# Kernel optimization log

Measured on AMD Instinct MI355X. Metric: run time of the kernel, lower is better.

Reference implementation:

```python
import jax, jax.numpy as jnp
import numpy as np

P = 7  # output_size


def _axis_weights(start, length, dim):
    """Per-roi 1D interpolation matrix A [R, P, dim] such that the roi_align
    output separates as out = Ay @ fm @ Ax^T (torchvision roi_align,
    aligned=False, sampling_ratio=-1 i.e. adaptive ceil(bin) samples)."""
    S = int(np.ceil(dim / P))  # max samples per bin (rois lie inside the image)
    bin_sz = length / P                               # [R]
    grid = jnp.ceil(length / P).astype(jnp.int32)     # adaptive samples per bin, [R]
    g = grid.astype(jnp.float32)[:, None, None]       # [R,1,1]
    s = jnp.arange(S, dtype=jnp.float32)              # [S]
    ph = jnp.arange(P, dtype=jnp.float32)             # [P]
    # sample coordinate: start + ph*bin + (s+0.5)*bin/grid  -> [R,P,S]
    coord = (start[:, None, None] + ph[None, :, None] * bin_sz[:, None, None]
             + (s[None, None, :] + 0.5) * bin_sz[:, None, None] / g)
    valid = (coord >= -1.0) & (coord <= dim)
    c = jnp.maximum(coord, 0.0)
    low = jnp.floor(c).astype(jnp.int32)
    hi_clamp = low >= dim - 1
    low = jnp.where(hi_clamp, dim - 1, low)
    high = jnp.where(hi_clamp, dim - 1, low + 1)
    cv = jnp.where(hi_clamp, low.astype(jnp.float32), c)
    l = cv - low.astype(jnp.float32)
    smask = (s[None, None, :] < g) & valid            # mask unused samples
    w = smask.astype(jnp.float32) / g                 # 1/count split per axis
    w_low = (1.0 - l) * w
    w_high = l * w
    R = start.shape[0]
    r_idx = jnp.arange(R)[:, None, None]
    p_idx = jnp.arange(P)[None, :, None]
    A = jnp.zeros((R, P, dim), dtype=jnp.float32)
    A = A.at[r_idx, p_idx, low].add(w_low)
    A = A.at[r_idx, p_idx, high].add(w_high)
    return A


def _roi_align(fm, rois):
    # fm: [C,H,W]; rois: [R,4] = (x1,y1,x2,y2); spatial_scale=1.0
    C, H, W = fm.shape
    x1, y1, x2, y2 = rois[:, 0], rois[:, 1], rois[:, 2], rois[:, 3]
    roi_w = jnp.maximum(x2 - x1, 1.0)
    roi_h = jnp.maximum(y2 - y1, 1.0)
    Ay = _axis_weights(y1, roi_h, H)                  # [R,P,H]
    Ax = _axis_weights(x1, roi_w, W)                  # [R,P,W]
    tmp = jnp.einsum('rph,chw->rcpw', Ay, fm)         # [R,C,P,W]
    return jnp.einsum('rcpw,rqw->rcpq', tmp, Ax)      # [R,C,P,P]


def _per_image(fm, b, g):
    # fm: [C,H,W], b: [N,4] boxes, g: [M,4] gt boxes
    N, M = b.shape[0], g.shape[0]
    # context boxes: union (min of mins, max of maxes) of every (box, gt) pair
    x1 = jnp.minimum(b[:, None, 0], g[None, :, 0])
    y1 = jnp.minimum(b[:, None, 1], g[None, :, 1])
    x2 = jnp.maximum(b[:, None, 2], g[None, :, 2])
    y2 = jnp.maximum(b[:, None, 3], g[None, :, 3])
    ctx = jnp.stack([x1, y1, x2, y2], axis=-1).reshape(N * M, 4)
    feats = _roi_align(fm, jnp.concatenate([b, ctx], axis=0))  # [N+N*M,C,P,P]
    box_f = feats[:N]
    ctx_mean = feats[N:].reshape(N, M, feats.shape[1], P, P).mean(axis=1)
    return box_f + ctx_mean                            # [N,C,P,P]


def setup_inputs() -> dict:
    key = jax.random.key(0)
    B, C, H, W, N, M = 2, 256, 56, 56, 64, 8
    k1, k2, k3, k4, k5 = jax.random.split(key, 5)
    feature_map = jax.random.normal(k1, (B, C, H, W), dtype=jnp.float32)
    # boxes inside the feature map, max side 0.35*H so adaptive grid <= ceil(H/7)
    b_xy1 = jax.random.uniform(k2, (B, N, 2), minval=0.0, maxval=0.64 * H)
    b_wh = jax.random.uniform(k3, (B, N, 2), minval=4.0, maxval=0.35 * H)
    boxes = jnp.concatenate([b_xy1, b_xy1 + b_wh], axis=-1).astype(jnp.float32)
    g_xy1 = jax.random.uniform(k4, (B, M, 2), minval=0.0, maxval=0.64 * H)
    g_wh = jax.random.uniform(k5, (B, M, 2), minval=4.0, maxval=0.35 * H)
    gt_boxes = jnp.concatenate([g_xy1, g_xy1 + g_wh], axis=-1).astype(jnp.float32)
    return {"feature_map": feature_map, "boxes": boxes, "gt_boxes": gt_boxes}


def reference(feature_map, boxes, gt_boxes):
    # returns [B, N, C, P, P] (stacked version of the per-image list output)
    return jax.vmap(_per_image)(feature_map, boxes, gt_boxes)
```

## Files before the change

### kernel.cpp

```cpp
#include <hip/hip_runtime.h>

#define B_ 2
#define C_ 256
#define H_ 56
#define W_ 56
#define N_ 64
#define M_ 8
#define P_ 7
#define R_ (N_ + N_*M_)
#define BR_ (B_*R_)
#define Y2_ (H_/2)
#define Y4_ (H_/4)
#define SCTX_ 4
#define JPN_ (1 + (M_)*SCTX_)
#define WROW_ 8

typedef _Float16 half2v __attribute__((ext_vector_type(2)));

#if __has_builtin(__builtin_amdgcn_fdot2)
#define FDOT2(a, b, c) __builtin_amdgcn_fdot2((a), (b), (c), false)
#else
static __device__ __forceinline__ float FDOT2(half2v a, half2v b, float c) {
    return fmaf((float)a.x, (float)b.x, fmaf((float)a.y, (float)b.y, c));
}
#endif

#define F_FMT4 0
#define N_FMT4 (B_*Y4_*W_*C_*2)
#define F_OUTS (F_FMT4 + N_FMT4)
#define N_OUTS (B_*N_*49*C_)
#define WS_ELEMS (F_OUTS + N_OUTS)

#define PREP_T (B_*Y4_*2)
#define PREP_N (PREP_T + 784)

__global__ __launch_bounds__(256) void k_prep(const float* __restrict__ fm,
                                              float* __restrict__ ws_f) {
    int bid = blockIdx.x;
    int tid = (int)threadIdx.x;

    if (bid < PREP_T) {
        int xh = bid & 1;
        int y4 = (bid >> 1) % Y4_;
        int b  = bid / (2 * Y4_);
        int c  = tid;
        int x0 = xh * (W_ / 2);
        const float* base = fm + (((size_t)b * C_ + c) * H_ + 4 * y4) * W_ + x0;
        const float4* r0 = (const float4*)(base);
        const float4* r1 = (const float4*)(base + W_);
        const float4* r2 = (const float4*)(base + 2 * W_);
        const float4* r3 = (const float4*)(base + 3 * W_);
        uint2* dst = (uint2*)ws_f + (((size_t)b * Y4_ + y4) * W_ + x0) * (size_t)C_ + c;
#pragma unroll
        for (int x4 = 0; x4 < W_ / 8; ++x4) {
            float4 a = r0[x4], e = r1[x4], f = r2[x4], g = r3[x4];
            half2v lo, hi; uint2 o;
            lo.x = (_Float16)a.x; lo.y = (_Float16)e.x;
            hi.x = (_Float16)f.x; hi.y = (_Float16)g.x;
            o.x = __builtin_bit_cast(unsigned int, lo);
            o.y = __builtin_bit_cast(unsigned int, hi);
            dst[(x4 * 4 + 0) * C_] = o;
            lo.x = (_Float16)a.y; lo.y = (_Float16)e.y;
            hi.x = (_Float16)f.y; hi.y = (_Float16)g.y;
            o.x = __builtin_bit_cast(unsigned int, lo);
            o.y = __builtin_bit_cast(unsigned int, hi);
            dst[(x4 * 4 + 1) * C_] = o;
            lo.x = (_Float16)a.z; lo.y = (_Float16)e.z;
            hi.x = (_Float16)f.z; hi.y = (_Float16)g.z;
            o.x = __builtin_bit_cast(unsigned int, lo);
            o.y = __builtin_bit_cast(unsigned int, hi);
            dst[(x4 * 4 + 2) * C_] = o;
            lo.x = (_Float16)a.w; lo.y = (_Float16)e.w;
            hi.x = (_Float16)f.w; hi.y = (_Float16)g.w;
            o.x = __builtin_bit_cast(unsigned int, lo);
            o.y = __builtin_bit_cast(unsigned int, hi);
            dst[(x4 * 4 + 3) * C_] = o;
        }
        return;
    }

    {
        int t = (bid - PREP_T) * 256 + tid;
        float4 z = {0.0f, 0.0f, 0.0f, 0.0f};
        float4* dst = (float4*)(ws_f + F_OUTS);
        dst[t * 2]     = z;
        dst[t * 2 + 1] = z;
    }
}

__global__ __launch_bounds__(256, 4) void k_main(const float* __restrict__ ws_f,
                                                 const float* __restrict__ boxes,
                                                 const float* __restrict__ gt,
                                                 float* __restrict__ outs) {
    __shared__ float        s_wyf[H_][WROW_];
    __shared__ unsigned int s_wy2[Y2_ * WROW_];
    __shared__ float        s_ax[W_][WROW_];

    int bid = blockIdx.x;
    int j   = bid % JPN_;
    int n   = (bid / JPN_) & (N_ - 1);
    int b   = bid / (JPN_ * N_);
    int k, s;
    if (j == 0) { k = 0; s = 0; }
    else        { k = 1 + ((j - 1) >> 2); s = (j - 1) & 3; }
    int tid  = (int)threadIdx.x;
    int lane = tid & 63;
    int rg   = tid >> 6;
    int c    = rg * 64 + lane;

    const float* bp = boxes + ((size_t)b * N_ + n) * 4;
    float bx1, by1, bx2, by2;
    if (k == 0) {
        bx1 = bp[0]; by1 = bp[1]; bx2 = bp[2]; by2 = bp[3];
    } else {
        const float* gp = gt + ((size_t)b * M_ + (k - 1)) * 4;
        bx1 = fminf(bp[0], gp[0]); by1 = fminf(bp[1], gp[1]);
        bx2 = fmaxf(bp[2], gp[2]); by2 = fmaxf(bp[3], gp[3]);
    }
    float rw = fmaxf(bx2 - bx1, 1.0f);
    float rh = fmaxf(by2 - by1, 1.0f);

    for (int e = tid; e < H_ * WROW_; e += 256) ((float*)s_wyf)[e] = 0.0f;
    for (int e = tid; e < W_ * WROW_; e += 256) ((float*)s_ax)[e] = 0.0f;
    __syncthreads();

    if (tid < P_) {
        int p = tid;
        float bin = rh / 7.0f;
        float gf  = ceilf(bin);
        int   g   = (int)gf;
        float ivg = 1.0f / gf;
        float start = by1 + (float)p * bin;
        for (int ss = 0; ss < g; ++ss) {
            float coord = start + ((float)ss + 0.5f) * bin * ivg;
            if (coord < -1.0f || coord > (float)H_) continue;
            float cc = fmaxf(coord, 0.0f);
            int low = (int)floorf(cc);
            int high; float l;
            if (low >= H_ - 1) { low = H_ - 1; high = H_ - 1; l = 0.0f; }
            else               { high = low + 1; l = cc - (float)low; }
            s_wyf[low][p]  += (1.0f - l) * ivg;
            s_wyf[high][p] += l * ivg;
        }
    } else if (tid >= 64 && tid < 64 + P_) {
        int p = tid - 64;
        float bin = rw / 7.0f;
        float gf  = ceilf(bin);
        int   g   = (int)gf;
        float ivg = 1.0f / gf;
        float fs  = (k == 0) ? ivg : ivg * (1.0f / (float)M_);
        float start = bx1 + (float)p * bin;
        for (int ss = 0; ss < g; ++ss) {
            float coord = start + ((float)ss + 0.5f) * bin * ivg;
            if (coord < -1.0f || coord > (float)W_) continue;
            float cc = fmaxf(coord, 0.0f);
            int low = (int)floorf(cc);
            int high; float l;
            if (low >= W_ - 1) { low = W_ - 1; high = W_ - 1; l = 0.0f; }
            else               { high = low + 1; l = cc - (float)low; }
            s_ax[low][p]  += (1.0f - l) * fs;
            s_ax[high][p] += l * fs;
        }
    }
    __syncthreads();

    if (tid < Y2_ * WROW_) {
        int q2 = tid >> 3, col = tid & 7;
        half2v h;
        if (col < P_) { h.x = (_Float16)s_wyf[2 * q2][col]; h.y = (_Float16)s_wyf[2 * q2 + 1][col]; }
        else          { h.x = (_Float16)0.0f; h.y = (_Float16)0.0f; }
        s_wy2[tid] = __builtin_bit_cast(unsigned int, h);
    }
    __syncthreads();

    int xlo = min(max((int)floorf(fmaxf(bx1, 0.0f)), 0), W_ - 1);
    int xhi = min(max((int)floorf(bx1 + rw) + 1, 0), W_ - 1) + 1;
    int ylo = min(max((int)floorf(fmaxf(by1, 0.0f)), 0), H_ - 1);
    int yhi = min(max((int)floorf(by1 + rh) + 1, 0), H_ - 1) + 1;
    int xs, xe;
    if (k == 0) { xs = xlo; xe = xhi; }
    else {
        int cw = (xhi - xlo + SCTX_ - 1) >> 2;
        xs = xlo + s * cw;
        xe = min(xs + cw, xhi);
    }
    if (xs >= xe) return;

    int ylo4 = ylo >> 2;
    int yhi4 = (yhi + 3) >> 2;

    const uint2* f4 = (const uint2*)ws_f + (size_t)b * (Y4_ * W_ * C_);

    float acc[49];
#pragma unroll
    for (int q = 0; q < 49; ++q) acc[q] = 0.0f;
    int live = 0;

    for (int x = xs; x < xe; x += 4) {
        float cs[4][P_];
#pragma unroll
        for (int i = 0; i < 4; ++i)
#pragma unroll
            for (int py = 0; py < P_; ++py) cs[i][py] = 0.0f;

        const uint2* cp = f4 + ((size_t)(ylo4 * W_ + x)) * C_ + c;
        for (int y4 = ylo4; y4 < yhi4; ++y4) {
            uint2 d0 = cp[0];
            uint2 d1 = cp[C_];
            uint2 d2 = cp[2 * C_];
            uint2 d3 = cp[3 * C_];
            uint4 wa0 = *(const uint4*)&s_wy2[(2 * y4) * WROW_];
            uint4 wb0 = *(const uint4*)&s_wy2[(2 * y4) * WROW_ + 4];
            uint4 wa1 = *(const uint4*)&s_wy2[(2 * y4 + 1) * WROW_];
            uint4 wb1 = *(const uint4*)&s_wy2[(2 * y4 + 1) * WROW_ + 4];
            half2v w0[7], w1[7];
            w0[0] = __builtin_bit_cast(half2v, wa0.x);
            w0[1] = __builtin_bit_cast(half2v, wa0.y);
            w0[2] = __builtin_bit_cast(half2v, wa0.z);
            w0[3] = __builtin_bit_cast(half2v, wa0.w);
            w0[4] = __builtin_bit_cast(half2v, wb0.x);
            w0[5] = __builtin_bit_cast(half2v, wb0.y);
            w0[6] = __builtin_bit_cast(half2v, wb0.z);
            w1[0] = __builtin_bit_cast(half2v, wa1.x);
            w1[1] = __builtin_bit_cast(half2v, wa1.y);
            w1[2] = __builtin_bit_cast(half2v, wa1.z);
            w1[3] = __builtin_bit_cast(half2v, wa1.w);
            w1[4] = __builtin_bit_cast(half2v, wb1.x);
            w1[5] = __builtin_bit_cast(half2v, wb1.y);
            w1[6] = __builtin_bit_cast(half2v, wb1.z);
            half2v v0a = __builtin_bit_cast(half2v, d0.x);
            half2v v0b = __builtin_bit_cast(half2v, d0.y);
            half2v v1a = __builtin_bit_cast(half2v, d1.x);
            half2v v1b = __builtin_bit_cast(half2v, d1.y);
            half2v v2a = __builtin_bit_cast(half2v, d2.x);
            half2v v2b = __builtin_bit_cast(half2v, d2.y);
            half2v v3a = __builtin_bit_cast(half2v, d3.x);
            half2v v3b = __builtin_bit_cast(half2v, d3.y);
#pragma unroll
            for (int py = 0; py < P_; ++py) {
                cs[0][py] = FDOT2(w1[py], v0b, FDOT2(w0[py], v0a, cs[0][py]));
                cs[1][py] = FDOT2(w1[py], v1b, FDOT2(w0[py], v1a, cs[1][py]));
                cs[2][py] = FDOT2(w1[py], v2b, FDOT2(w0[py], v2a, cs[2][py]));
                cs[3][py] = FDOT2(w1[py], v3b, FDOT2(w0[py], v3a, cs[3][py]));
            }
            cp += W_ * C_;
        }

#pragma unroll
        for (int i = 0; i < 4; ++i) {
            if (x + i < xe) {
                float av[8];
                *(float4*)(&av[0]) = *(const float4*)&s_ax[x + i][0];
                *(float4*)(&av[4]) = *(const float4*)&s_ax[x + i][4];
#pragma unroll
                for (int px = 0; px < P_; ++px) {
                    float w = av[px];
                    if (w != 0.0f) {
                        live |= 1 << px;
#pragma unroll
                        for (int py = 0; py < P_; ++py)
                            acc[py * P_ + px] = fmaf(w, cs[i][py], acc[py * P_ + px]);
                    }
                }
            }
        }
    }

    float* os = outs + ((size_t)b * N_ + n) * (49 * C_) + c;
#pragma unroll
    for (int px = 0; px < P_; ++px) {
        if (live & (1 << px)) {
#pragma unroll
            for (int py = 0; py < P_; ++py)
                atomicAdd(os + (py * P_ + px) * C_, acc[py * P_ + px]);
        }
    }
}

__global__ __launch_bounds__(256) void k_final(const float* __restrict__ outs,
                                               float* __restrict__ out) {
    __shared__ float t[49 * 257];
    int bn  = blockIdx.x;
    int tid = (int)threadIdx.x;
    const float* src = outs + (size_t)bn * (49 * C_);
    for (int e = tid; e < 49 * C_; e += 256) {
        int q = e >> 8, c = e & 255;
        t[q * 257 + c] = src[e];
    }
    __syncthreads();
    float* dst = out + (size_t)bn * (C_ * 49);
    for (int e = tid; e < C_ * 49; e += 256) {
        int c = e / 49, q = e % 49;
        dst[e] = t[q * 257 + c];
    }
}

extern "C" void kernel_launch(void* const* d_in, const int* in_sizes, int n_in,
                              void* d_out, int out_size, void* d_ws, size_t ws_size,
                              hipStream_t stream) {
    const float* fm    = (const float*)d_in[0];
    const float* boxes = (const float*)d_in[1];
    const float* gt    = (const float*)d_in[2];
    float* ws_f = (float*)d_ws;
    float* out  = (float*)d_out;
    float* outs = ws_f + F_OUTS;

    k_prep<<<PREP_N, 256, 0, stream>>>(fm, ws_f);
    k_main<<<B_ * N_ * JPN_, 256, 0, stream>>>(ws_f, boxes, gt, outs);
    k_final<<<B_ * N_, 256, 0, stream>>>(outs, out);
}
```

Measured before the change: 149.8 us.

## Use persistent work-stealing main kernel and finer-grained prep and final kernels

The main kernel becomes a persistent grid of 2048 blocks that pull job indices from a global atomic counter, which is reset in the prep kernel. The per-roi weight build now spreads the sample loop over 8 threads per output bin using shared-memory atomics. The prep kernel is split into 7 x-chunks per row group, and the final transpose is split into 4 channel groups per roi, to raise parallelism in both. The aim is better load balance across uneven roi sizes and less launch tail, at the cost of atomic-counter contention and extra block-level syncs per job.

```diff
diff --git a/kernel.cpp b/kernel.cpp
--- a/kernel.cpp
+++ b/kernel.cpp
@@ -13,6 +13,8 @@
 #define Y4_ (H_/4)
 #define SCTX_ 4
 #define JPN_ (1 + (M_)*SCTX_)
+#define NJOBS_ (B_*N_*JPN_)
+#define PERSIST_ 2048
 #define WROW_ 8
 
 typedef _Float16 half2v __attribute__((ext_vector_type(2)));
@@ -29,9 +31,10 @@
 #define N_FMT4 (B_*Y4_*W_*C_*2)
 #define F_OUTS (F_FMT4 + N_FMT4)
 #define N_OUTS (B_*N_*49*C_)
-#define WS_ELEMS (F_OUTS + N_OUTS)
-
-#define PREP_T (B_*Y4_*2)
+#define F_CNT  (F_OUTS + N_OUTS)
+#define WS_ELEMS (F_CNT + 64)
+
+#define PREP_T (B_*Y4_*7)
 #define PREP_N (PREP_T + 784)
 
 __global__ __launch_bounds__(256) void k_prep(const float* __restrict__ fm,
@@ -40,47 +43,40 @@
     int tid = (int)threadIdx.x;
 
     if (bid < PREP_T) {
-        int xh = bid & 1;
-        int y4 = (bid >> 1) % Y4_;
-        int b  = bid / (2 * Y4_);
+        int xc = bid % 7;
+        int y4 = (bid / 7) % Y4_;
+        int b  = bid / (7 * Y4_);
         int c  = tid;
-        int x0 = xh * (W_ / 2);
+        int x0 = xc * 8;
         const float* base = fm + (((size_t)b * C_ + c) * H_ + 4 * y4) * W_ + x0;
-        const float4* r0 = (const float4*)(base);
-        const float4* r1 = (const float4*)(base + W_);
-        const float4* r2 = (const float4*)(base + 2 * W_);
-        const float4* r3 = (const float4*)(base + 3 * W_);
+        float4 a0 = *(const float4*)(base);
+        float4 a1 = *(const float4*)(base + 4);
+        float4 e0 = *(const float4*)(base + W_);
+        float4 e1 = *(const float4*)(base + W_ + 4);
+        float4 f0 = *(const float4*)(base + 2 * W_);
+        float4 f1 = *(const float4*)(base + 2 * W_ + 4);
+        float4 g0 = *(const float4*)(base + 3 * W_);
+        float4 g1 = *(const float4*)(base + 3 * W_ + 4);
+        float r0[8] = {a0.x, a0.y, a0.z, a0.w, a1.x, a1.y, a1.z, a1.w};
+        float r1[8] = {e0.x, e0.y, e0.z, e0.w, e1.x, e1.y, e1.z, e1.w};
+        float r2[8] = {f0.x, f0.y, f0.z, f0.w, f1.x, f1.y, f1.z, f1.w};
+        float r3[8] = {g0.x, g0.y, g0.z, g0.w, g1.x, g1.y, g1.z, g1.w};
         uint2* dst = (uint2*)ws_f + (((size_t)b * Y4_ + y4) * W_ + x0) * (size_t)C_ + c;
 #pragma unroll
-        for (int x4 = 0; x4 < W_ / 8; ++x4) {
-            float4 a = r0[x4], e = r1[x4], f = r2[x4], g = r3[x4];
+        for (int xi = 0; xi < 8; ++xi) {
             half2v lo, hi; uint2 o;
-            lo.x = (_Float16)a.x; lo.y = (_Float16)e.x;
-            hi.x = (_Float16)f.x; hi.y = (_Float16)g.x;
+            lo.x = (_Float16)r0[xi]; lo.y = (_Float16)r1[xi];
+            hi.x = (_Float16)r2[xi]; hi.y = (_Float16)r3[xi];
             o.x = __builtin_bit_cast(unsigned int, lo);
             o.y = __builtin_bit_cast(unsigned int, hi);
-            dst[(x4 * 4 + 0) * C_] = o;
-            lo.x = (_Float16)a.y; lo.y = (_Float16)e.y;
-            hi.x = (_Float16)f.y; hi.y = (_Float16)g.y;
-            o.x = __builtin_bit_cast(unsigned int, lo);
-            o.y = __builtin_bit_cast(unsigned int, hi);
-            dst[(x4 * 4 + 1) * C_] = o;
-            lo.x = (_Float16)a.z; lo.y = (_Float16)e.z;
-            hi.x = (_Float16)f.z; hi.y = (_Float16)g.z;
-            o.x = __builtin_bit_cast(unsigned int, lo);
-            o.y = __builtin_bit_cast(unsigned int, hi);
-            dst[(x4 * 4 + 2) * C_] = o;
-            lo.x = (_Float16)a.w; lo.y = (_Float16)e.w;
-            hi.x = (_Float16)f.w; hi.y = (_Float16)g.w;
-            o.x = __builtin_bit_cast(unsigned int, lo);
-            o.y = __builtin_bit_cast(unsigned int, hi);
-            dst[(x4 * 4 + 3) * C_] = o;
+            dst[xi * C_] = o;
         }
         return;
     }
 
     {
         int t = (bid - PREP_T) * 256 + tid;
+        if (t == 0) *(int*)(ws_f + F_CNT) = 0;
         float4 z = {0.0f, 0.0f, 0.0f, 0.0f};
         float4* dst = (float4*)(ws_f + F_OUTS);
         dst[t * 2]     = z;
@@ -91,207 +87,222 @@
 __global__ __launch_bounds__(256, 4) void k_main(const float* __restrict__ ws_f,
                                                  const float* __restrict__ boxes,
                                                  const float* __restrict__ gt,
-                                                 float* __restrict__ outs) {
+                                                 float* __restrict__ outs,
+                                                 int* cnt) {
     __shared__ float        s_wyf[H_][WROW_];
     __shared__ unsigned int s_wy2[Y2_ * WROW_];
     __shared__ float        s_ax[W_][WROW_];
-
-    int bid = blockIdx.x;
-    int j   = bid % JPN_;
-    int n   = (bid / JPN_) & (N_ - 1);
-    int b   = bid / (JPN_ * N_);
-    int k, s;
-    if (j == 0) { k = 0; s = 0; }
-    else        { k = 1 + ((j - 1) >> 2); s = (j - 1) & 3; }
+    __shared__ int          s_job;
+
     int tid  = (int)threadIdx.x;
-    int lane = tid & 63;
-    int rg   = tid >> 6;
-    int c    = rg * 64 + lane;
-
-    const float* bp = boxes + ((size_t)b * N_ + n) * 4;
-    float bx1, by1, bx2, by2;
-    if (k == 0) {
-        bx1 = bp[0]; by1 = bp[1]; bx2 = bp[2]; by2 = bp[3];
-    } else {
-        const float* gp = gt + ((size_t)b * M_ + (k - 1)) * 4;
-        bx1 = fminf(bp[0], gp[0]); by1 = fminf(bp[1], gp[1]);
-        bx2 = fmaxf(bp[2], gp[2]); by2 = fmaxf(bp[3], gp[3]);
-    }
-    float rw = fmaxf(bx2 - bx1, 1.0f);
-    float rh = fmaxf(by2 - by1, 1.0f);
-
-    for (int e = tid; e < H_ * WROW_; e += 256) ((float*)s_wyf)[e] = 0.0f;
-    for (int e = tid; e < W_ * WROW_; e += 256) ((float*)s_ax)[e] = 0.0f;
-    __syncthreads();
-
-    if (tid < P_) {
-        int p = tid;
-        float bin = rh / 7.0f;
-        float gf  = ceilf(bin);
-        int   g   = (int)gf;
-        float ivg = 1.0f / gf;
-        float start = by1 + (float)p * bin;
-        for (int ss = 0; ss < g; ++ss) {
-            float coord = start + ((float)ss + 0.5f) * bin * ivg;
-            if (coord < -1.0f || coord > (float)H_) continue;
-            float cc = fmaxf(coord, 0.0f);
-            int low = (int)floorf(cc);
-            int high; float l;
-            if (low >= H_ - 1) { low = H_ - 1; high = H_ - 1; l = 0.0f; }
-            else               { high = low + 1; l = cc - (float)low; }
-            s_wyf[low][p]  += (1.0f - l) * ivg;
-            s_wyf[high][p] += l * ivg;
-        }
-    } else if (tid >= 64 && tid < 64 + P_) {
-        int p = tid - 64;
-        float bin = rw / 7.0f;
-        float gf  = ceilf(bin);
-        int   g   = (int)gf;
-        float ivg = 1.0f / gf;
-        float fs  = (k == 0) ? ivg : ivg * (1.0f / (float)M_);
-        float start = bx1 + (float)p * bin;
-        for (int ss = 0; ss < g; ++ss) {
-            float coord = start + ((float)ss + 0.5f) * bin * ivg;
-            if (coord < -1.0f || coord > (float)W_) continue;
-            float cc = fmaxf(coord, 0.0f);
-            int low = (int)floorf(cc);
-            int high; float l;
-            if (low >= W_ - 1) { low = W_ - 1; high = W_ - 1; l = 0.0f; }
-            else               { high = low + 1; l = cc - (float)low; }
-            s_ax[low][p]  += (1.0f - l) * fs;
-            s_ax[high][p] += l * fs;
-        }
-    }
-    __syncthreads();
-
-    if (tid < Y2_ * WROW_) {
-        int q2 = tid >> 3, col = tid & 7;
-        half2v h;
-        if (col < P_) { h.x = (_Float16)s_wyf[2 * q2][col]; h.y = (_Float16)s_wyf[2 * q2 + 1][col]; }
-        else          { h.x = (_Float16)0.0f; h.y = (_Float16)0.0f; }
-        s_wy2[tid] = __builtin_bit_cast(unsigned int, h);
-    }
-    __syncthreads();
-
-    int xlo = min(max((int)floorf(fmaxf(bx1, 0.0f)), 0), W_ - 1);
-    int xhi = min(max((int)floorf(bx1 + rw) + 1, 0), W_ - 1) + 1;
-    int ylo = min(max((int)floorf(fmaxf(by1, 0.0f)), 0), H_ - 1);
-    int yhi = min(max((int)floorf(by1 + rh) + 1, 0), H_ - 1) + 1;
-    int xs, xe;
-    if (k == 0) { xs = xlo; xe = xhi; }
-    else {
-        int cw = (xhi - xlo + SCTX_ - 1) >> 2;
-        xs = xlo + s * cw;
-        xe = min(xs + cw, xhi);
-    }
-    if (xs >= xe) return;
-
-    int ylo4 = ylo >> 2;
-    int yhi4 = (yhi + 3) >> 2;
-
-    const uint2* f4 = (const uint2*)ws_f + (size_t)b * (Y4_ * W_ * C_);
-
-    float acc[49];
-#pragma unroll
-    for (int q = 0; q < 49; ++q) acc[q] = 0.0f;
-    int live = 0;
-
-    for (int x = xs; x < xe; x += 4) {
-        float cs[4][P_];
-#pragma unroll
-        for (int i = 0; i < 4; ++i)
-#pragma unroll
-            for (int py = 0; py < P_; ++py) cs[i][py] = 0.0f;
-
-        const uint2* cp = f4 + ((size_t)(ylo4 * W_ + x)) * C_ + c;
-        for (int y4 = ylo4; y4 < yhi4; ++y4) {
-            uint2 d0 = cp[0];
-            uint2 d1 = cp[C_];
-            uint2 d2 = cp[2 * C_];
-            uint2 d3 = cp[3 * C_];
-            uint4 wa0 = *(const uint4*)&s_wy2[(2 * y4) * WROW_];
-            uint4 wb0 = *(const uint4*)&s_wy2[(2 * y4) * WROW_ + 4];
-            uint4 wa1 = *(const uint4*)&s_wy2[(2 * y4 + 1) * WROW_];
-            uint4 wb1 = *(const uint4*)&s_wy2[(2 * y4 + 1) * WROW_ + 4];
-            half2v w0[7], w1[7];
-            w0[0] = __builtin_bit_cast(half2v, wa0.x);
-            w0[1] = __builtin_bit_cast(half2v, wa0.y);
-            w0[2] = __builtin_bit_cast(half2v, wa0.z);
-            w0[3] = __builtin_bit_cast(half2v, wa0.w);
-            w0[4] = __builtin_bit_cast(half2v, wb0.x);
-            w0[5] = __builtin_bit_cast(half2v, wb0.y);
-            w0[6] = __builtin_bit_cast(half2v, wb0.z);
-            w1[0] = __builtin_bit_cast(half2v, wa1.x);
-            w1[1] = __builtin_bit_cast(half2v, wa1.y);
-            w1[2] = __builtin_bit_cast(half2v, wa1.z);
-            w1[3] = __builtin_bit_cast(half2v, wa1.w);
-            w1[4] = __builtin_bit_cast(half2v, wb1.x);
-            w1[5] = __builtin_bit_cast(half2v, wb1.y);
-            w1[6] = __builtin_bit_cast(half2v, wb1.z);
-            half2v v0a = __builtin_bit_cast(half2v, d0.x);
-            half2v v0b = __builtin_bit_cast(half2v, d0.y);
-            half2v v1a = __builtin_bit_cast(half2v, d1.x);
-            half2v v1b = __builtin_bit_cast(half2v, d1.y);
-            half2v v2a = __builtin_bit_cast(half2v, d2.x);
-            half2v v2b = __builtin_bit_cast(half2v, d2.y);
-            half2v v3a = __builtin_bit_cast(half2v, d3.x);
-            half2v v3b = __builtin_bit_cast(half2v, d3.y);
-#pragma unroll
-            for (int py = 0; py < P_; ++py) {
-                cs[0][py] = FDOT2(w1[py], v0b, FDOT2(w0[py], v0a, cs[0][py]));
-                cs[1][py] = FDOT2(w1[py], v1b, FDOT2(w0[py], v1a, cs[1][py]));
-                cs[2][py] = FDOT2(w1[py], v2b, FDOT2(w0[py], v2a, cs[2][py]));
-                cs[3][py] = FDOT2(w1[py], v3b, FDOT2(w0[py], v3a, cs[3][py]));
-            }
-            cp += W_ * C_;
-        }
-
-#pragma unroll
-        for (int i = 0; i < 4; ++i) {
-            if (x + i < xe) {
-                float av[8];
-                *(float4*)(&av[0]) = *(const float4*)&s_ax[x + i][0];
-                *(float4*)(&av[4]) = *(const float4*)&s_ax[x + i][4];
-#pragma unroll
-                for (int px = 0; px < P_; ++px) {
-                    float w = av[px];
-                    if (w != 0.0f) {
-                        live |= 1 << px;
-#pragma unroll
-                        for (int py = 0; py < P_; ++py)
-                            acc[py * P_ + px] = fmaf(w, cs[i][py], acc[py * P_ + px]);
+    int c    = tid;
+
+    for (;;) {
+        __syncthreads();
+        if (tid == 0) s_job = atomicAdd(cnt, 1);
+        __syncthreads();
+        int bid = s_job;
+        if (bid >= NJOBS_) return;
+
+        int j = bid % JPN_;
+        int n = (bid / JPN_) & (N_ - 1);
+        int b = bid / (JPN_ * N_);
+        int k, s;
+        if (j == 0) { k = 0; s = 0; }
+        else        { k = 1 + ((j - 1) >> 2); s = (j - 1) & 3; }
+
+        const float* bp = boxes + ((size_t)b * N_ + n) * 4;
+        float bx1, by1, bx2, by2;
+        if (k == 0) {
+            bx1 = bp[0]; by1 = bp[1]; bx2 = bp[2]; by2 = bp[3];
+        } else {
+            const float* gp = gt + ((size_t)b * M_ + (k - 1)) * 4;
+            bx1 = fminf(bp[0], gp[0]); by1 = fminf(bp[1], gp[1]);
+            bx2 = fmaxf(bp[2], gp[2]); by2 = fmaxf(bp[3], gp[3]);
+        }
+        float rw = fmaxf(bx2 - bx1, 1.0f);
+        float rh = fmaxf(by2 - by1, 1.0f);
+
+        for (int e = tid; e < H_ * WROW_; e += 256) ((float*)s_wyf)[e] = 0.0f;
+        for (int e = tid; e < W_ * WROW_; e += 256) ((float*)s_ax)[e] = 0.0f;
+        __syncthreads();
+
+        if (tid < 64) {
+            int p = tid >> 3, ss0 = tid & 7;
+            if (p < P_) {
+                float bin = rh / 7.0f;
+                float gf  = ceilf(bin);
+                int   g   = (int)gf;
+                float ivg = 1.0f / gf;
+                float start = by1 + (float)p * bin;
+                for (int ss = ss0; ss < g; ss += 8) {
+                    float coord = start + ((float)ss + 0.5f) * bin * ivg;
+                    if (coord < -1.0f || coord > (float)H_) continue;
+                    float cc = fmaxf(coord, 0.0f);
+                    int low = (int)floorf(cc);
+                    int high; float l;
+                    if (low >= H_ - 1) { low = H_ - 1; high = H_ - 1; l = 0.0f; }
+                    else               { high = low + 1; l = cc - (float)low; }
+                    atomicAdd(&s_wyf[low][p],  (1.0f - l) * ivg);
+                    atomicAdd(&s_wyf[high][p], l * ivg);
+                }
+            }
+        } else if (tid < 128) {
+            int t = tid - 64;
+            int p = t >> 3, ss0 = t & 7;
+            if (p < P_) {
+                float bin = rw / 7.0f;
+                float gf  = ceilf(bin);
+                int   g   = (int)gf;
+                float ivg = 1.0f / gf;
+                float fs  = (k == 0) ? ivg : ivg * (1.0f / (float)M_);
+                float start = bx1 + (float)p * bin;
+                for (int ss = ss0; ss < g; ss += 8) {
+                    float coord = start + ((float)ss + 0.5f) * bin * ivg;
+                    if (coord < -1.0f || coord > (float)W_) continue;
+                    float cc = fmaxf(coord, 0.0f);
+                    int low = (int)floorf(cc);
+                    int high; float l;
+                    if (low >= W_ - 1) { low = W_ - 1; high = W_ - 1; l = 0.0f; }
+                    else               { high = low + 1; l = cc - (float)low; }
+                    atomicAdd(&s_ax[low][p],  (1.0f - l) * fs);
+                    atomicAdd(&s_ax[high][p], l * fs);
+                }
+            }
+        }
+        __syncthreads();
+
+        if (tid < Y2_ * WROW_) {
+            int q2 = tid >> 3, col = tid & 7;
+            half2v h;
+            if (col < P_) { h.x = (_Float16)s_wyf[2 * q2][col]; h.y = (_Float16)s_wyf[2 * q2 + 1][col]; }
+            else          { h.x = (_Float16)0.0f; h.y = (_Float16)0.0f; }
+            s_wy2[tid] = __builtin_bit_cast(unsigned int, h);
+        }
+        __syncthreads();
+
+        int xlo = min(max((int)floorf(fmaxf(bx1, 0.0f)), 0), W_ - 1);
+        int xhi = min(max((int)floorf(bx1 + rw) + 1, 0), W_ - 1) + 1;
+        int ylo = min(max((int)floorf(fmaxf(by1, 0.0f)), 0), H_ - 1);
+        int yhi = min(max((int)floorf(by1 + rh) + 1, 0), H_ - 1) + 1;
+        int xs, xe;
+        if (k == 0) { xs = xlo; xe = xhi; }
+        else {
+            int cw = (xhi - xlo + SCTX_ - 1) >> 2;
+            xs = xlo + s * cw;
+            xe = min(xs + cw, xhi);
+        }
+        if (xs >= xe) continue;
+
+        int ylo4 = ylo >> 2;
+        int yhi4 = (yhi + 3) >> 2;
+
+        const uint2* f4 = (const uint2*)ws_f + (size_t)b * (Y4_ * W_ * C_);
+
+        float acc[49];
+#pragma unroll
+        for (int q = 0; q < 49; ++q) acc[q] = 0.0f;
+        int live = 0;
+
+        for (int x = xs; x < xe; x += 4) {
+            float cs[4][P_];
+#pragma unroll
+            for (int i = 0; i < 4; ++i)
+#pragma unroll
+                for (int py = 0; py < P_; ++py) cs[i][py] = 0.0f;
+
+            const uint2* cp = f4 + ((size_t)(ylo4 * W_ + x)) * C_ + c;
+            for (int y4 = ylo4; y4 < yhi4; ++y4) {
+                uint2 d0 = cp[0];
+                uint2 d1 = cp[C_];
+                uint2 d2 = cp[2 * C_];
+                uint2 d3 = cp[3 * C_];
+                uint4 wa0 = *(const uint4*)&s_wy2[(2 * y4) * WROW_];
+                uint4 wb0 = *(const uint4*)&s_wy2[(2 * y4) * WROW_ + 4];
+                uint4 wa1 = *(const uint4*)&s_wy2[(2 * y4 + 1) * WROW_];
+                uint4 wb1 = *(const uint4*)&s_wy2[(2 * y4 + 1) * WROW_ + 4];
+                half2v w0[7], w1[7];
+                w0[0] = __builtin_bit_cast(half2v, wa0.x);
+                w0[1] = __builtin_bit_cast(half2v, wa0.y);
+                w0[2] = __builtin_bit_cast(half2v, wa0.z);
+                w0[3] = __builtin_bit_cast(half2v, wa0.w);
+                w0[4] = __builtin_bit_cast(half2v, wb0.x);
+                w0[5] = __builtin_bit_cast(half2v, wb0.y);
+                w0[6] = __builtin_bit_cast(half2v, wb0.z);
+                w1[0] = __builtin_bit_cast(half2v, wa1.x);
+                w1[1] = __builtin_bit_cast(half2v, wa1.y);
+                w1[2] = __builtin_bit_cast(half2v, wa1.z);
+                w1[3] = __builtin_bit_cast(half2v, wa1.w);
+                w1[4] = __builtin_bit_cast(half2v, wb1.x);
+                w1[5] = __builtin_bit_cast(half2v, wb1.y);
+                w1[6] = __builtin_bit_cast(half2v, wb1.z);
+                half2v v0a = __builtin_bit_cast(half2v, d0.x);
+                half2v v0b = __builtin_bit_cast(half2v, d0.y);
+                half2v v1a = __builtin_bit_cast(half2v, d1.x);
+                half2v v1b = __builtin_bit_cast(half2v, d1.y);
+                half2v v2a = __builtin_bit_cast(half2v, d2.x);
+                half2v v2b = __builtin_bit_cast(half2v, d2.y);
+                half2v v3a = __builtin_bit_cast(half2v, d3.x);
+                half2v v3b = __builtin_bit_cast(half2v, d3.y);
+#pragma unroll
+                for (int py = 0; py < P_; ++py) {
+                    cs[0][py] = FDOT2(w1[py], v0b, FDOT2(w0[py], v0a, cs[0][py]));
+                    cs[1][py] = FDOT2(w1[py], v1b, FDOT2(w0[py], v1a, cs[1][py]));
+                    cs[2][py] = FDOT2(w1[py], v2b, FDOT2(w0[py], v2a, cs[2][py]));
+                    cs[3][py] = FDOT2(w1[py], v3b, FDOT2(w0[py], v3a, cs[3][py]));
+                }
+                cp += W_ * C_;
+            }
+
+#pragma unroll
+            for (int i = 0; i < 4; ++i) {
+                if (x + i < xe) {
+                    float av[8];
+                    *(float4*)(&av[0]) = *(const float4*)&s_ax[x + i][0];
+                    *(float4*)(&av[4]) = *(const float4*)&s_ax[x + i][4];
+#pragma unroll
+                    for (int px = 0; px < P_; ++px) {
+                        float w = av[px];
+                        if (w != 0.0f) {
+                            live |= 1 << px;
+#pragma unroll
+                            for (int py = 0; py < P_; ++py)
+                                acc[py * P_ + px] = fmaf(w, cs[i][py], acc[py * P_ + px]);
+                        }
                     }
                 }
             }
         }
-    }
-
-    float* os = outs + ((size_t)b * N_ + n) * (49 * C_) + c;
-#pragma unroll
-    for (int px = 0; px < P_; ++px) {
-        if (live & (1 << px)) {
-#pragma unroll
-            for (int py = 0; py < P_; ++py)
-                atomicAdd(os + (py * P_ + px) * C_, acc[py * P_ + px]);
+
+        float* os = outs + ((size_t)b * N_ + n) * (49 * C_) + c;
+#pragma unroll
+        for (int px = 0; px < P_; ++px) {
+            if (live & (1 << px)) {
+#pragma unroll
+                for (int py = 0; py < P_; ++py)
+                    atomicAdd(os + (py * P_ + px) * C_, acc[py * P_ + px]);
+            }
         }
     }
 }
 
 __global__ __launch_bounds__(256) void k_final(const float* __restrict__ outs,
                                                float* __restrict__ out) {
-    __shared__ float t[49 * 257];
-    int bn  = blockIdx.x;
+    __shared__ float t[49 * 65];
+    int bid = blockIdx.x;
+    int cg  = bid & 3;
+    int bn  = bid >> 2;
     int tid = (int)threadIdx.x;
-    const float* src = outs + (size_t)bn * (49 * C_);
-    for (int e = tid; e < 49 * C_; e += 256) {
-        int q = e >> 8, c = e & 255;
-        t[q * 257 + c] = src[e];
+    const float* src = outs + (size_t)bn * (49 * C_) + cg * 64;
+    for (int e = tid; e < 49 * 64; e += 256) {
+        int q = e >> 6, c = e & 63;
+        t[q * 65 + c] = src[q * C_ + c];
     }
     __syncthreads();
-    float* dst = out + (size_t)bn * (C_ * 49);
-    for (int e = tid; e < C_ * 49; e += 256) {
-        int c = e / 49, q = e % 49;
-        dst[e] = t[q * 257 + c];
+    float* dst = out + (size_t)bn * (C_ * 49) + (size_t)cg * 64 * 49;
+    for (int e = tid; e < 64 * 49; e += 256) {
+        int c = e / 49, q = e - c * 49;
+        dst[e] = t[q * 65 + c];
     }
 }
 
@@ -304,8 +315,9 @@
     float* ws_f = (float*)d_ws;
     float* out  = (float*)d_out;
     float* outs = ws_f + F_OUTS;
+    int*   cnt  = (int*)(ws_f + F_CNT);
 
     k_prep<<<PREP_N, 256, 0, stream>>>(fm, ws_f);
-    k_main<<<B_ * N_ * JPN_, 256, 0, stream>>>(ws_f, boxes, gt, outs);
-    k_final<<<B_ * N_, 256, 0, stream>>>(outs, out);
-}
+    k_main<<<PERSIST_, 256, 0, stream>>>(ws_f, boxes, gt, outs, cnt);
+    k_final<<<B_ * N_ * 4, 256, 0, stream>>>(outs, out);
+}
```

Result: slower. 184.4 us (+23.1%).

## Split context work by output column bins, transpose prep via LDS, split final

Applied to the files above, without the earlier changes.

The prep kernel now stages a 64-channel by 4-row by 28-column tile in shared memory so that both its global reads and its fp16 writes are coalesced, and it launches four times as many blocks. The context-box work split changes from equal x-column chunks to pairs of output column bins: each split zeros the Ax weights outside its bins and restricts its x range to those bins, which is meant to cut redundant atomics and wasted FMAs. The final transpose kernel is split into four channel groups to raise parallelism. The risk is that the per-bin x range computed from bin edges may miss bilinear neighbours at the edges, and the extra shared-memory traffic adds cost.

```diff
diff --git a/kernel.cpp b/kernel.cpp
--- a/kernel.cpp
+++ b/kernel.cpp
@@ -7,8 +7,6 @@
 #define N_ 64
 #define M_ 8
 #define P_ 7
-#define R_ (N_ + N_*M_)
-#define BR_ (B_*R_)
 #define Y2_ (H_/2)
 #define Y4_ (H_/4)
 #define SCTX_ 4
@@ -31,60 +29,48 @@
 #define N_OUTS (B_*N_*49*C_)
 #define WS_ELEMS (F_OUTS + N_OUTS)
 
-#define PREP_T (B_*Y4_*2)
+#define PREP_T (B_*Y4_*4*2)
 #define PREP_N (PREP_T + 784)
 
 __global__ __launch_bounds__(256) void k_prep(const float* __restrict__ fm,
                                               float* __restrict__ ws_f) {
+    __shared__ float t[28 * 257 + 8];
     int bid = blockIdx.x;
     int tid = (int)threadIdx.x;
 
     if (bid < PREP_T) {
         int xh = bid & 1;
-        int y4 = (bid >> 1) % Y4_;
-        int b  = bid / (2 * Y4_);
-        int c  = tid;
-        int x0 = xh * (W_ / 2);
-        const float* base = fm + (((size_t)b * C_ + c) * H_ + 4 * y4) * W_ + x0;
-        const float4* r0 = (const float4*)(base);
-        const float4* r1 = (const float4*)(base + W_);
-        const float4* r2 = (const float4*)(base + 2 * W_);
-        const float4* r3 = (const float4*)(base + 3 * W_);
-        uint2* dst = (uint2*)ws_f + (((size_t)b * Y4_ + y4) * W_ + x0) * (size_t)C_ + c;
-#pragma unroll
-        for (int x4 = 0; x4 < W_ / 8; ++x4) {
-            float4 a = r0[x4], e = r1[x4], f = r2[x4], g = r3[x4];
+        int cg = (bid >> 1) & 3;
+        int y4 = (bid >> 3) % Y4_;
+        int b  = (bid >> 3) / Y4_;
+        int c0 = cg * 64, x0 = xh * 28;
+        for (int e = tid; e < 64 * 4 * 28; e += 256) {
+            int c_l = e / 112, rem = e % 112;
+            int y_l = rem / 28, x_l = rem % 28;
+            t[x_l * 257 + y_l * 64 + c_l] =
+                fm[(((size_t)b * C_ + c0 + c_l) * H_ + 4 * y4 + y_l) * W_ + x0 + x_l];
+        }
+        __syncthreads();
+        uint2* dst = (uint2*)ws_f;
+        for (int e = tid; e < 28 * 64; e += 256) {
+            int x_l = e >> 6, c_l = e & 63;
+            const float* p = &t[x_l * 257 + c_l];
             half2v lo, hi; uint2 o;
-            lo.x = (_Float16)a.x; lo.y = (_Float16)e.x;
-            hi.x = (_Float16)f.x; hi.y = (_Float16)g.x;
+            lo.x = (_Float16)p[0];   lo.y = (_Float16)p[64];
+            hi.x = (_Float16)p[128]; hi.y = (_Float16)p[192];
             o.x = __builtin_bit_cast(unsigned int, lo);
             o.y = __builtin_bit_cast(unsigned int, hi);
-            dst[(x4 * 4 + 0) * C_] = o;
-            lo.x = (_Float16)a.y; lo.y = (_Float16)e.y;
-            hi.x = (_Float16)f.y; hi.y = (_Float16)g.y;
-            o.x = __builtin_bit_cast(unsigned int, lo);
-            o.y = __builtin_bit_cast(unsigned int, hi);
-            dst[(x4 * 4 + 1) * C_] = o;
-            lo.x = (_Float16)a.z; lo.y = (_Float16)e.z;
-            hi.x = (_Float16)f.z; hi.y = (_Float16)g.z;
-            o.x = __builtin_bit_cast(unsigned int, lo);
-            o.y = __builtin_bit_cast(unsigned int, hi);
-            dst[(x4 * 4 + 2) * C_] = o;
-            lo.x = (_Float16)a.w; lo.y = (_Float16)e.w;
-            hi.x = (_Float16)f.w; hi.y = (_Float16)g.w;
-            o.x = __builtin_bit_cast(unsigned int, lo);
-            o.y = __builtin_bit_cast(unsigned int, hi);
-            dst[(x4 * 4 + 3) * C_] = o;
+            dst[(((size_t)b * Y4_ + y4) * W_ + x0 + x_l) * (size_t)C_ + c0 + c_l] = o;
         }
         return;
     }
 
     {
-        int t = (bid - PREP_T) * 256 + tid;
+        int tz = (bid - PREP_T) * 256 + tid;
         float4 z = {0.0f, 0.0f, 0.0f, 0.0f};
         float4* dst = (float4*)(ws_f + F_OUTS);
-        dst[t * 2]     = z;
-        dst[t * 2 + 1] = z;
+        dst[tz * 2]     = z;
+        dst[tz * 2 + 1] = z;
     }
 }
 
@@ -103,10 +89,11 @@
     int k, s;
     if (j == 0) { k = 0; s = 0; }
     else        { k = 1 + ((j - 1) >> 2); s = (j - 1) & 3; }
+    int p0, p1;
+    if (k == 0) { p0 = 0; p1 = P_ - 1; }
+    else        { p0 = 2 * s; p1 = (2 * s + 1 < P_) ? 2 * s + 1 : P_ - 1; }
     int tid  = (int)threadIdx.x;
-    int lane = tid & 63;
-    int rg   = tid >> 6;
-    int c    = rg * 64 + lane;
+    int c    = tid;
 
     const float* bp = boxes + ((size_t)b * N_ + n) * 4;
     float bx1, by1, bx2, by2;
@@ -170,22 +157,33 @@
         if (col < P_) { h.x = (_Float16)s_wyf[2 * q2][col]; h.y = (_Float16)s_wyf[2 * q2 + 1][col]; }
         else          { h.x = (_Float16)0.0f; h.y = (_Float16)0.0f; }
         s_wy2[tid] = __builtin_bit_cast(unsigned int, h);
+    } else if (k != 0) {
+        int r = tid - 224;
+#pragma unroll
+        for (int px = 0; px < P_; ++px) {
+            if (px < p0 || px > p1) {
+                s_ax[r][px] = 0.0f;
+                if (r + 32 < W_) s_ax[r + 32][px] = 0.0f;
+            }
+        }
     }
     __syncthreads();
 
-    int xlo = min(max((int)floorf(fmaxf(bx1, 0.0f)), 0), W_ - 1);
-    int xhi = min(max((int)floorf(bx1 + rw) + 1, 0), W_ - 1) + 1;
+    int xs, xe;
+    if (k == 0) {
+        xs = min(max((int)floorf(fmaxf(bx1, 0.0f)), 0), W_ - 1);
+        xe = min(max((int)floorf(bx1 + rw) + 1, 0), W_ - 1) + 1;
+    } else {
+        float binw = rw * (1.0f / 7.0f);
+        float lo_f = bx1 + (float)p0 * binw;
+        float hi_f = bx1 + (float)(p1 + 1) * binw;
+        xs = min(max((int)floorf(fmaxf(lo_f, 0.0f)), 0), W_ - 1);
+        xe = min(max((int)floorf(fminf(hi_f, (float)W_)) + 1, 0), W_ - 1) + 1;
+    }
+    if (xs >= xe) return;
+
     int ylo = min(max((int)floorf(fmaxf(by1, 0.0f)), 0), H_ - 1);
     int yhi = min(max((int)floorf(by1 + rh) + 1, 0), H_ - 1) + 1;
-    int xs, xe;
-    if (k == 0) { xs = xlo; xe = xhi; }
-    else {
-        int cw = (xhi - xlo + SCTX_ - 1) >> 2;
-        xs = xlo + s * cw;
-        xe = min(xs + cw, xhi);
-    }
-    if (xs >= xe) return;
-
     int ylo4 = ylo >> 2;
     int yhi4 = (yhi + 3) >> 2;
 
@@ -279,19 +277,21 @@
 
 __global__ __launch_bounds__(256) void k_final(const float* __restrict__ outs,
                                                float* __restrict__ out) {
-    __shared__ float t[49 * 257];
-    int bn  = blockIdx.x;
+    __shared__ float t[49 * 65];
+    int bid = blockIdx.x;
+    int cg  = bid & 3;
+    int bn  = bid >> 2;
     int tid = (int)threadIdx.x;
-    const float* src = outs + (size_t)bn * (49 * C_);
-    for (int e = tid; e < 49 * C_; e += 256) {
-        int q = e >> 8, c = e & 255;
-        t[q * 257 + c] = src[e];
+    const float* src = outs + (size_t)bn * (49 * C_) + cg * 64;
+    for (int e = tid; e < 49 * 64; e += 256) {
+        int q = e >> 6, c = e & 63;
+        t[q * 65 + c] = src[q * C_ + c];
     }
     __syncthreads();
-    float* dst = out + (size_t)bn * (C_ * 49);
-    for (int e = tid; e < C_ * 49; e += 256) {
-        int c = e / 49, q = e % 49;
-        dst[e] = t[q * 257 + c];
+    float* dst = out + (size_t)bn * (C_ * 49) + (size_t)cg * 64 * 49;
+    for (int e = tid; e < 64 * 49; e += 256) {
+        int c = e / 49, q = e - c * 49;
+        dst[e] = t[q * 65 + c];
     }
 }
 
@@ -307,5 +307,5 @@
 
     k_prep<<<PREP_N, 256, 0, stream>>>(fm, ws_f);
     k_main<<<B_ * N_ * JPN_, 256, 0, stream>>>(ws_f, boxes, gt, outs);
-    k_final<<<B_ * N_, 256, 0, stream>>>(outs, out);
-}
+    k_final<<<B_ * N_ * 4, 256, 0, stream>>>(outs, out);
+}
```

New measurement: 149.7 us. About the same (-0.1%).
